# Optimization experiments

Hardware: AMD Instinct MI355X
Metric: run time of the kernel (lower is better)

Reference implementation:

```python
import jax, jax.numpy as jnp
import numpy as np


def setup_inputs() -> dict:
    key = jax.random.key(0)
    ks = jax.random.split(key, 5)
    B, C, D, H, W = 2, 256, 8, 28, 28
    mid = C // 2
    # Kaiming-normal-ish init (std = sqrt(2/fan_in)) for 1x1 conv weights
    def kaiming(k, shape, fan_in):
        return jax.random.normal(k, shape, dtype=jnp.float32) * np.sqrt(2.0 / fan_in)
    x = jax.random.normal(ks[0], (B, C, D, H, W), dtype=jnp.float32)
    w1 = kaiming(ks[1], (mid, C), C)
    w2 = kaiming(ks[2], (mid, C), C)
    w3 = kaiming(ks[3], (mid, C), C)
    w4 = kaiming(ks[4], (C, mid), mid)
    b1 = jnp.zeros((mid,), jnp.float32)
    b2 = jnp.zeros((mid,), jnp.float32)
    b3 = jnp.zeros((mid,), jnp.float32)
    b4 = jnp.zeros((C,), jnp.float32)
    return {"x": x, "w1": w1, "b1": b1, "w2": w2, "b2": b2,
            "w3": w3, "b3": b3, "w4": w4, "b4": b4}


def reference(x, w1, b1, w2, b2, w3, b3, w4, b4):
    # x: [B, C, D, H, W]; 1x1x1 Conv3d == channel matmul over flattened N = D*H*W
    B, C, D, H, W = x.shape
    N = D * H * W
    xf = x.reshape(B, C, N)                                   # [B, C, N]
    # theta: conv1 -> [B, N, mid]
    e1 = jnp.einsum('mc,bcn->bnm', w1, xf) + b1               # [B, N, mid]
    # phi: conv2 -> [B, mid, N]
    e2 = jnp.einsum('mc,bcn->bmn', w2, xf) + b2[:, None]      # [B, mid, N]
    # g: conv3 -> [B, N, mid]
    e3 = jnp.einsum('mc,bcn->bnm', w3, xf) + b3               # [B, N, mid]
    # unscaled attention: softmax over keys (last axis)
    kernel = jnp.einsum('bnm,bmk->bnk', e1, e2)               # [B, N, N]
    kernel = jax.nn.softmax(kernel, axis=2)
    attn = jnp.einsum('bnk,bkm->bnm', kernel, e3)             # [B, N, mid]
    # conv4 (1x1 Conv1d): mid -> C, applied on [B, mid, N]
    y = jnp.einsum('cm,bnm->bcn', w4, attn) + b4[:, None]     # [B, C, N]
    return x + y.reshape(B, C, D, H, W)
```

## Files before the change

### kernel.cpp

```cpp
#include <hip/hip_runtime.h>


#define BB  2
#define CC  256
#define NN  6272
#define MID 128

typedef _Float16 half4_t __attribute__((ext_vector_type(4)));
typedef _Float16 half8_t __attribute__((ext_vector_type(8)));
typedef float    floatx16 __attribute__((ext_vector_type(16)));

__device__ __forceinline__ void fma4(float4& a, const float4 v, const float s) {
    a.x += v.x * s; a.y += v.y * s; a.z += v.z * s; a.w += v.w * s;
}
__device__ __forceinline__ float dot4(const float4 a, const float4 b) {
    return a.x * b.x + a.y * b.y + a.z * b.z + a.w * b.w;
}

__global__ __launch_bounds__(256, 2) void proj_kernel(
    const float* __restrict__ x,
    const float* __restrict__ w1, const float* __restrict__ bi1,
    const float* __restrict__ w2, const float* __restrict__ bi2,
    const float* __restrict__ w3, const float* __restrict__ bi3,
    _Float16* __restrict__ Qg, _Float16* __restrict__ Kg, _Float16* __restrict__ VtG)
{
    const int t  = threadIdx.x;
    const int n0 = blockIdx.x * 64;
    const int pj = blockIdx.y;
    const int b  = blockIdx.z;
    const float* w  = (pj == 0) ? w1 : (pj == 1) ? w2 : w3;
    const float* bi = (pj == 0) ? bi1 : (pj == 1) ? bi2 : bi3;

    __shared__ float xs[CC * 68];
    {
        const float* xb = x + (size_t)b * CC * NN;
        for (int r = t; r < CC * 16; r += 256) {
            int c = r >> 4, j = (r & 15) << 2;
            float4 v = *(const float4*)(xb + (size_t)c * NN + n0 + j);
            *(float4*)&xs[c * 68 + j] = v;
        }
    }
    __syncthreads();

    const int n4 = (t & 15) << 2;
    const int m0 = (t >> 4) << 3;
    float4 acc4[8];
    #pragma unroll
    for (int k = 0; k < 8; ++k) acc4[k] = make_float4(0.f, 0.f, 0.f, 0.f);

    for (int cc = 0; cc < CC; cc += 4) {
        float4 xv[4];
        #pragma unroll
        for (int u = 0; u < 4; ++u)
            xv[u] = *(const float4*)&xs[(cc + u) * 68 + n4];
        #pragma unroll
        for (int k = 0; k < 8; ++k) {
            float4 wq = *(const float4*)(w + (size_t)(m0 + k) * CC + cc);
            fma4(acc4[k], xv[0], wq.x);
            fma4(acc4[k], xv[1], wq.y);
            fma4(acc4[k], xv[2], wq.z);
            fma4(acc4[k], xv[3], wq.w);
        }
    }

    const float* af = (const float*)acc4;
    float bb[8];
    #pragma unroll
    for (int k = 0; k < 8; ++k) bb[k] = bi[m0 + k];

    if (pj < 2) {
        _Float16* eo = ((pj == 0) ? Qg : Kg) + (size_t)b * NN * MID;
        #pragma unroll
        for (int i = 0; i < 4; ++i) {
            half8_t h;
            #pragma unroll
            for (int k = 0; k < 8; ++k) h[k] = (_Float16)(af[k * 4 + i] + bb[k]);
            *(half8_t*)(eo + (size_t)(n0 + n4 + i) * MID + m0) = h;
        }
    } else {
        _Float16* eo = VtG + (size_t)b * MID * NN;
        #pragma unroll
        for (int k = 0; k < 8; ++k) {
            half4_t h;
            #pragma unroll
            for (int i = 0; i < 4; ++i) h[i] = (_Float16)(af[k * 4 + i] + bb[k]);
            *(half4_t*)(eo + (size_t)(m0 + k) * NN + n0 + n4) = h;
        }
    }
}

__global__ __launch_bounds__(128, 2) void attn_kernel(
    const _Float16* __restrict__ Qg, const _Float16* __restrict__ Kg,
    const _Float16* __restrict__ VtG, float* __restrict__ attnW)
{
    const int t    = threadIdx.x;
    const int lane = t & 63;
    const int wave = t >> 6;
    const int l31  = lane & 31;
    const int l5   = lane >> 5;
    const int q0   = blockIdx.x * 32;
    const int b    = blockIdx.y;

    __shared__ __align__(16) char lds[40960];
    _Float16* Ks = (_Float16*)lds;
    _Float16* Vt = (_Float16*)(lds + 17408);
    _Float16* Pt = (_Float16*)(lds + 17408 + 18432);
    float* stats = (float*)(lds + 40448);
    float* Obuf  = (float*)lds;

    const _Float16* Qb = Qg + ((size_t)b * NN + q0) * MID;
    const _Float16* Kb = Kg + (size_t)b * NN * MID;
    const _Float16* Vb = VtG + (size_t)b * MID * NN;

    half8_t qf[8];
    #pragma unroll
    for (int ds = 0; ds < 8; ++ds)
        qf[ds] = *(const half8_t*)(Qb + (size_t)l31 * MID + ds * 16 + l5 * 8);

    floatx16 o[4];
    #pragma unroll
    for (int dt = 0; dt < 4; ++dt)
        #pragma unroll
        for (int j = 0; j < 16; ++j) o[dt][j] = 0.f;
    float m_run = -3.0e38f, l_run = 0.f;

    for (int kt = 0; kt < NN / 64; ++kt) {
        const int nk = kt * 64;
        #pragma unroll
        for (int it = 0; it < 8; ++it) {
            int c = it * 128 + t;
            int r = c >> 4, off = (c & 15) * 8;
            *(half8_t*)(Ks + r * 136 + off) =
                *(const half8_t*)(Kb + (size_t)(nk + r) * MID + off);
        }
        #pragma unroll
        for (int it = 0; it < 8; ++it) {
            int c = it * 128 + t;
            int d = c >> 3, off = (c & 7) * 8;
            *(half8_t*)(Vt + d * 72 + off) =
                *(const half8_t*)(Vb + (size_t)d * NN + nk + off);
        }
        __syncthreads();

        floatx16 s;
        #pragma unroll
        for (int j = 0; j < 16; ++j) s[j] = 0.f;
        const _Float16* krow = Ks + (wave * 32 + l31) * 136 + l5 * 8;
        #pragma unroll
        for (int ds = 0; ds < 8; ++ds)
            s = __builtin_amdgcn_mfma_f32_32x32x16_f16(
                    *(const half8_t*)(krow + ds * 16), qf[ds], s, 0, 0, 0);

        float tmax = s[0];
        #pragma unroll
        for (int j = 1; j < 16; ++j) tmax = fmaxf(tmax, s[j]);
        tmax = fmaxf(tmax, __shfl_xor(tmax, 32));
        const float m_new = fmaxf(m_run, tmax);
        const float alpha = __expf(m_run - m_new);
        m_run = m_new;

        float psum = 0.f;
        _Float16* prow = Pt + l31 * 72 + wave * 32 + 4 * l5;
        #pragma unroll
        for (int g = 0; g < 4; ++g) {
            float p0 = __expf(s[4 * g + 0] - m_new);
            float p1 = __expf(s[4 * g + 1] - m_new);
            float p2 = __expf(s[4 * g + 2] - m_new);
            float p3 = __expf(s[4 * g + 3] - m_new);
            psum += (p0 + p1) + (p2 + p3);
            half4_t h;
            h[0] = (_Float16)p0; h[1] = (_Float16)p1;
            h[2] = (_Float16)p2; h[3] = (_Float16)p3;
            *(half4_t*)(prow + 8 * g) = h;
        }
        psum += __shfl_xor(psum, 32);
        l_run = l_run * alpha + psum;

        #pragma unroll
        for (int dt = 0; dt < 4; ++dt)
            #pragma unroll
            for (int j = 0; j < 16; ++j) o[dt][j] *= alpha;

        __builtin_amdgcn_s_waitcnt(0xC07F);

        #pragma unroll
        for (int ks = 0; ks < 2; ++ks) {
            half8_t pf = *(const half8_t*)(Pt + l31 * 72 + wave * 32 + ks * 16 + l5 * 8);
            const _Float16* vcol = Vt + wave * 32 + ks * 16 + l5 * 8;
            #pragma unroll
            for (int dt = 0; dt < 4; ++dt)
                o[dt] = __builtin_amdgcn_mfma_f32_32x32x16_f16(
                            *(const half8_t*)(vcol + (dt * 32 + l31) * 72), pf,
                            o[dt], 0, 0, 0);
        }
        __syncthreads();
    }

    if (l5 == 0) {
        stats[wave * 64 + l31]      = m_run;
        stats[wave * 64 + 32 + l31] = l_run;
    }
    __syncthreads();
    const float m_o  = stats[(1 ^ wave) * 64 + l31];
    const float l_o  = stats[(1 ^ wave) * 64 + 32 + l31];
    const float m_st = fmaxf(m_run, m_o);
    const float sc   = __expf(m_run - m_st);
    const float l_st = l_run * sc + l_o * __expf(m_o - m_st);
    const float inv  = 1.0f / l_st;

    if (wave == 1) {
        #pragma unroll
        for (int dt = 0; dt < 4; ++dt)
            #pragma unroll
            for (int j = 0; j < 16; ++j) {
                int d = dt * 32 + (j & 3) + 8 * (j >> 2) + 4 * l5;
                Obuf[l31 * 132 + d] = o[dt][j] * sc;
            }
    }
    __syncthreads();
    if (wave == 0) {
        #pragma unroll
        for (int dt = 0; dt < 4; ++dt)
            #pragma unroll
            for (int j = 0; j < 16; ++j) {
                int d = dt * 32 + (j & 3) + 8 * (j >> 2) + 4 * l5;
                Obuf[l31 * 132 + d] = (Obuf[l31 * 132 + d] + o[dt][j] * sc) * inv;
            }
    }
    __syncthreads();
    #pragma unroll
    for (int it = 0; it < 8; ++it) {
        int c = it * 128 + t;
        int q = c >> 5, off = (c & 31) * 4;
        *(float4*)(attnW + ((size_t)b * NN + q0 + q) * MID + off) =
            *(const float4*)(Obuf + q * 132 + off);
    }
}

__global__ __launch_bounds__(256, 2) void epi_kernel(
    const float* __restrict__ attnW, const float* __restrict__ w4,
    const float* __restrict__ b4, const float* __restrict__ x,
    float* __restrict__ out)
{
    const int t  = threadIdx.x;
    const int n0 = blockIdx.x * 64;
    const int b  = blockIdx.y;

    __shared__ float as[64 * 132];
    for (int r = t; r < 64 * 32; r += 256) {
        int q = r >> 5, g = r & 31;
        float4 v = *(const float4*)(attnW + ((size_t)b * NN + (n0 + q)) * MID + (g << 2));
        *(float4*)&as[q * 132 + (g << 2)] = v;
    }
    __syncthreads();

    const int n4 = (t & 15) << 2;
    const int c0 = (t >> 4) << 4;
    float4 accE[16];
    #pragma unroll
    for (int k = 0; k < 16; ++k) accE[k] = make_float4(0.f, 0.f, 0.f, 0.f);

    for (int ms = 0; ms < 32; ++ms) {
        float4 av[4];
        #pragma unroll
        for (int i = 0; i < 4; ++i)
            av[i] = *(const float4*)&as[(n4 + i) * 132 + (ms << 2)];
        #pragma unroll
        for (int k = 0; k < 16; ++k) {
            float4 wq = *(const float4*)(w4 + (size_t)(c0 + k) * MID + (ms << 2));
            accE[k].x += dot4(av[0], wq);
            accE[k].y += dot4(av[1], wq);
            accE[k].z += dot4(av[2], wq);
            accE[k].w += dot4(av[3], wq);
        }
    }

    #pragma unroll
    for (int k = 0; k < 16; ++k) {
        const int c = c0 + k;
        const float bv = b4[c];
        const size_t off = ((size_t)b * CC + c) * NN + n0 + n4;
        float4 xr = *(const float4*)(x + off);
        float4 r;
        r.x = accE[k].x + bv + xr.x;
        r.y = accE[k].y + bv + xr.y;
        r.z = accE[k].z + bv + xr.z;
        r.w = accE[k].w + bv + xr.w;
        *(float4*)(out + off) = r;
    }
}

extern "C" void kernel_launch(void* const* d_in, const int* in_sizes, int n_in,
                              void* d_out, int out_size, void* d_ws, size_t ws_size,
                              hipStream_t stream)
{
    const float* x  = (const float*)d_in[0];
    const float* w1 = (const float*)d_in[1];
    const float* b1 = (const float*)d_in[2];
    const float* w2 = (const float*)d_in[3];
    const float* b2 = (const float*)d_in[4];
    const float* w3 = (const float*)d_in[5];
    const float* b3 = (const float*)d_in[6];
    const float* w4 = (const float*)d_in[7];
    const float* b4 = (const float*)d_in[8];
    float* out = (float*)d_out;

    _Float16* Qg  = (_Float16*)d_ws;
    _Float16* Kg  = Qg + (size_t)BB * NN * MID;
    _Float16* VtG = Kg + (size_t)BB * NN * MID;
    float* attnW  = (float*)(VtG + (size_t)BB * NN * MID);

    proj_kernel<<<dim3(NN / 64, 3, BB), 256, 0, stream>>>(x, w1, b1, w2, b2, w3, b3, Qg, Kg, VtG);
    attn_kernel<<<dim3(NN / 32, BB), 128, 0, stream>>>(Qg, Kg, VtG, attnW);
    epi_kernel<<<dim3(NN / 64, BB), 256, 0, stream>>>(attnW, w4, b4, x, out);
}
```

Baseline: 306.8 us.

## Split attention keys across blocks with a combine kernel and fp16 intermediates

Splits the key dimension of the attention kernel into four chunks, so the grid has four times as many blocks, and writes fp16 partial outputs plus per-row max and sum stats. A new combine kernel merges the partials. K is now read straight from global memory instead of through LDS, which shrinks LDS use so occupancy can rise, and the V/P LDS strides change. It also skips the rescale of the accumulator when the running max does not change, and stores the attention output in fp16 for the epilogue. This adds an extra kernel, the partial-output traffic (staged in the output buffer) and some fp16 rounding.

```diff
diff --git a/kernel.cpp b/kernel.cpp
--- a/kernel.cpp
+++ b/kernel.cpp
@@ -5,6 +5,8 @@
 #define CC  256
 #define NN  6272
 #define MID 128
+#define KS  4
+#define NT  (NN / 64)
 
 typedef _Float16 half4_t __attribute__((ext_vector_type(4)));
 typedef _Float16 half8_t __attribute__((ext_vector_type(8)));
@@ -89,9 +91,10 @@
     }
 }
 
-__global__ __launch_bounds__(128, 2) void attn_kernel(
+__global__ __launch_bounds__(128, 4) void attn_kernel(
     const _Float16* __restrict__ Qg, const _Float16* __restrict__ Kg,
-    const _Float16* __restrict__ VtG, float* __restrict__ attnW)
+    const _Float16* __restrict__ VtG, _Float16* __restrict__ Opart,
+    float* __restrict__ MLg)
 {
     const int t    = threadIdx.x;
     const int lane = t & 63;
@@ -99,13 +102,15 @@
     const int l31  = lane & 31;
     const int l5   = lane >> 5;
     const int q0   = blockIdx.x * 32;
-    const int b    = blockIdx.y;
-
-    __shared__ __align__(16) char lds[40960];
-    _Float16* Ks = (_Float16*)lds;
-    _Float16* Vt = (_Float16*)(lds + 17408);
-    _Float16* Pt = (_Float16*)(lds + 17408 + 18432);
-    float* stats = (float*)(lds + 40448);
+    const int sp   = blockIdx.y;
+    const int b    = blockIdx.z;
+    const int kt0  = (NT * sp) / KS;
+    const int kt1  = (NT * (sp + 1)) / KS;
+
+    __shared__ __align__(16) char lds[22272];
+    _Float16* Vt = (_Float16*)lds;
+    _Float16* Pt = (_Float16*)(lds + 17408);
+    float* stats = (float*)(lds + 21760);
     float* Obuf  = (float*)lds;
 
     const _Float16* Qb = Qg + ((size_t)b * NN + q0) * MID;
@@ -124,20 +129,13 @@
         for (int j = 0; j < 16; ++j) o[dt][j] = 0.f;
     float m_run = -3.0e38f, l_run = 0.f;
 
-    for (int kt = 0; kt < NN / 64; ++kt) {
+    for (int kt = kt0; kt < kt1; ++kt) {
         const int nk = kt * 64;
-        #pragma unroll
-        for (int it = 0; it < 8; ++it) {
-            int c = it * 128 + t;
-            int r = c >> 4, off = (c & 15) * 8;
-            *(half8_t*)(Ks + r * 136 + off) =
-                *(const half8_t*)(Kb + (size_t)(nk + r) * MID + off);
-        }
         #pragma unroll
         for (int it = 0; it < 8; ++it) {
             int c = it * 128 + t;
             int d = c >> 3, off = (c & 7) * 8;
-            *(half8_t*)(Vt + d * 72 + off) =
+            *(half8_t*)(Vt + d * 68 + off) =
                 *(const half8_t*)(Vb + (size_t)d * NN + nk + off);
         }
         __syncthreads();
@@ -145,7 +143,7 @@
         floatx16 s;
         #pragma unroll
         for (int j = 0; j < 16; ++j) s[j] = 0.f;
-        const _Float16* krow = Ks + (wave * 32 + l31) * 136 + l5 * 8;
+        const _Float16* krow = Kb + (size_t)(nk + wave * 32 + l31) * MID + l5 * 8;
         #pragma unroll
         for (int ds = 0; ds < 8; ++ds)
             s = __builtin_amdgcn_mfma_f32_32x32x16_f16(
@@ -155,18 +153,26 @@
         #pragma unroll
         for (int j = 1; j < 16; ++j) tmax = fmaxf(tmax, s[j]);
         tmax = fmaxf(tmax, __shfl_xor(tmax, 32));
-        const float m_new = fmaxf(m_run, tmax);
-        const float alpha = __expf(m_run - m_new);
-        m_run = m_new;
+
+        if (!__all(tmax <= m_run)) {
+            const float m_new = fmaxf(m_run, tmax);
+            const float alpha = __expf(m_run - m_new);
+            m_run = m_new;
+            l_run *= alpha;
+            #pragma unroll
+            for (int dt = 0; dt < 4; ++dt)
+                #pragma unroll
+                for (int j = 0; j < 16; ++j) o[dt][j] *= alpha;
+        }
 
         float psum = 0.f;
-        _Float16* prow = Pt + l31 * 72 + wave * 32 + 4 * l5;
+        _Float16* prow = Pt + l31 * 68 + wave * 32 + 4 * l5;
         #pragma unroll
         for (int g = 0; g < 4; ++g) {
-            float p0 = __expf(s[4 * g + 0] - m_new);
-            float p1 = __expf(s[4 * g + 1] - m_new);
-            float p2 = __expf(s[4 * g + 2] - m_new);
-            float p3 = __expf(s[4 * g + 3] - m_new);
+            float p0 = __expf(s[4 * g + 0] - m_run);
+            float p1 = __expf(s[4 * g + 1] - m_run);
+            float p2 = __expf(s[4 * g + 2] - m_run);
+            float p3 = __expf(s[4 * g + 3] - m_run);
             psum += (p0 + p1) + (p2 + p3);
             half4_t h;
             h[0] = (_Float16)p0; h[1] = (_Float16)p1;
@@ -174,23 +180,18 @@
             *(half4_t*)(prow + 8 * g) = h;
         }
         psum += __shfl_xor(psum, 32);
-        l_run = l_run * alpha + psum;
-
-        #pragma unroll
-        for (int dt = 0; dt < 4; ++dt)
-            #pragma unroll
-            for (int j = 0; j < 16; ++j) o[dt][j] *= alpha;
+        l_run += psum;
 
         __builtin_amdgcn_s_waitcnt(0xC07F);
 
         #pragma unroll
         for (int ks = 0; ks < 2; ++ks) {
-            half8_t pf = *(const half8_t*)(Pt + l31 * 72 + wave * 32 + ks * 16 + l5 * 8);
+            half8_t pf = *(const half8_t*)(Pt + l31 * 68 + wave * 32 + ks * 16 + l5 * 8);
             const _Float16* vcol = Vt + wave * 32 + ks * 16 + l5 * 8;
             #pragma unroll
             for (int dt = 0; dt < 4; ++dt)
                 o[dt] = __builtin_amdgcn_mfma_f32_32x32x16_f16(
-                            *(const half8_t*)(vcol + (dt * 32 + l31) * 72), pf,
+                            *(const half8_t*)(vcol + (dt * 32 + l31) * 68), pf,
                             o[dt], 0, 0, 0);
         }
         __syncthreads();
@@ -206,7 +207,12 @@
     const float m_st = fmaxf(m_run, m_o);
     const float sc   = __expf(m_run - m_st);
     const float l_st = l_run * sc + l_o * __expf(m_o - m_st);
-    const float inv  = 1.0f / l_st;
+
+    if (t < 32) {
+        float* mlb = MLg + ((size_t)(b * KS + sp) * 2) * NN + q0;
+        mlb[t]      = m_st;
+        mlb[NN + t] = l_st;
+    }
 
     if (wave == 1) {
         #pragma unroll
@@ -224,21 +230,71 @@
             #pragma unroll
             for (int j = 0; j < 16; ++j) {
                 int d = dt * 32 + (j & 3) + 8 * (j >> 2) + 4 * l5;
-                Obuf[l31 * 132 + d] = (Obuf[l31 * 132 + d] + o[dt][j] * sc) * inv;
+                Obuf[l31 * 132 + d] += o[dt][j] * sc;
             }
     }
     __syncthreads();
-    #pragma unroll
-    for (int it = 0; it < 8; ++it) {
+    _Float16* Ob = Opart + ((size_t)(b * KS + sp) * NN + q0) * MID;
+    #pragma unroll
+    for (int it = 0; it < 4; ++it) {
         int c = it * 128 + t;
-        int q = c >> 5, off = (c & 31) * 4;
-        *(float4*)(attnW + ((size_t)b * NN + q0 + q) * MID + off) =
-            *(const float4*)(Obuf + q * 132 + off);
-    }
+        int q = c >> 4, g = c & 15;
+        const float* src = &Obuf[q * 132 + g * 8];
+        half8_t h;
+        #pragma unroll
+        for (int j = 0; j < 8; ++j) h[j] = (_Float16)src[j];
+        *(half8_t*)(Ob + (size_t)q * MID + g * 8) = h;
+    }
+}
+
+__global__ __launch_bounds__(256, 4) void comb_kernel(
+    const _Float16* __restrict__ Opart, const float* __restrict__ MLg,
+    _Float16* __restrict__ attnW)
+{
+    const int t  = threadIdx.x;
+    const int b  = blockIdx.y;
+    const int q  = blockIdx.x * 32 + (t >> 3);
+    const int dg = (t & 7) * 16;
+
+    float mv[KS], lv[KS];
+    float m_g = -3.0e38f;
+    #pragma unroll
+    for (int s = 0; s < KS; ++s) {
+        const float* mlb = MLg + ((size_t)(b * KS + s) * 2) * NN;
+        mv[s] = mlb[q];
+        lv[s] = mlb[NN + q];
+        m_g = fmaxf(m_g, mv[s]);
+    }
+    float lg = 0.f, w[KS];
+    #pragma unroll
+    for (int s = 0; s < KS; ++s) { w[s] = __expf(mv[s] - m_g); lg += lv[s] * w[s]; }
+    const float inv = 1.0f / lg;
+
+    float acc[16];
+    #pragma unroll
+    for (int j = 0; j < 16; ++j) acc[j] = 0.f;
+    #pragma unroll
+    for (int s = 0; s < KS; ++s) {
+        const half8_t* Op = (const half8_t*)(Opart + ((size_t)(b * KS + s) * NN + q) * MID + dg);
+        half8_t v0 = Op[0], v1 = Op[1];
+        #pragma unroll
+        for (int j = 0; j < 8; ++j) {
+            acc[j]     += (float)v0[j] * w[s];
+            acc[8 + j] += (float)v1[j] * w[s];
+        }
+    }
+    half8_t h0, h1;
+    #pragma unroll
+    for (int j = 0; j < 8; ++j) {
+        h0[j] = (_Float16)(acc[j] * inv);
+        h1[j] = (_Float16)(acc[8 + j] * inv);
+    }
+    half8_t* Ow = (half8_t*)(attnW + ((size_t)b * NN + q) * MID + dg);
+    Ow[0] = h0; Ow[1] = h1;
 }
 
 __global__ __launch_bounds__(256, 2) void epi_kernel(
-    const float* __restrict__ attnW, const float* __restrict__ w4,
+    const _Float16* __restrict__ attnW, const float* __restrict__ w4,
     const float* __restrict__ b4, const float* __restrict__ x,
     float* __restrict__ out)
 {
@@ -247,10 +303,12 @@
     const int b  = blockIdx.y;
 
     __shared__ float as[64 * 132];
-    for (int r = t; r < 64 * 32; r += 256) {
-        int q = r >> 5, g = r & 31;
-        float4 v = *(const float4*)(attnW + ((size_t)b * NN + (n0 + q)) * MID + (g << 2));
-        *(float4*)&as[q * 132 + (g << 2)] = v;
+    for (int r = t; r < 64 * 16; r += 256) {
+        int q = r >> 4, g = r & 15;
+        half8_t v = *(const half8_t*)(attnW + ((size_t)b * NN + n0 + q) * MID + g * 8);
+        float* dst = &as[q * 132 + g * 8];
+        #pragma unroll
+        for (int j = 0; j < 8; ++j) dst[j] = (float)v[j];
     }
     __syncthreads();
 
@@ -305,12 +363,15 @@
     const float* b4 = (const float*)d_in[8];
     float* out = (float*)d_out;
 
-    _Float16* Qg  = (_Float16*)d_ws;
-    _Float16* Kg  = Qg + (size_t)BB * NN * MID;
-    _Float16* VtG = Kg + (size_t)BB * NN * MID;
-    float* attnW  = (float*)(VtG + (size_t)BB * NN * MID);
+    _Float16* Qg    = (_Float16*)d_ws;
+    _Float16* Kg    = Qg + (size_t)BB * NN * MID;
+    _Float16* VtG   = Kg + (size_t)BB * NN * MID;
+    _Float16* attnW = VtG + (size_t)BB * NN * MID;
+    float* MLg      = (float*)(attnW + (size_t)BB * NN * MID);
+    _Float16* Opart = (_Float16*)d_out;
 
     proj_kernel<<<dim3(NN / 64, 3, BB), 256, 0, stream>>>(x, w1, b1, w2, b2, w3, b3, Qg, Kg, VtG);
-    attn_kernel<<<dim3(NN / 32, BB), 128, 0, stream>>>(Qg, Kg, VtG, attnW);
+    attn_kernel<<<dim3(NN / 32, KS, BB), 128, 0, stream>>>(Qg, Kg, VtG, Opart, MLg);
+    comb_kernel<<<dim3(NN / 32, BB), 256, 0, stream>>>(Opart, MLg, attnW);
     epi_kernel<<<dim3(NN / 64, BB), 256, 0, stream>>>(attnW, w4, b4, x, out);
 }
```

Measured after the change: 385.1 us. +25.5%, slower.

## Prefetch next K/V tile into registers and pad LDS strides

Applied to the files above, without the earlier changes.

Global loads of the next K and V tiles are issued into registers before the current tile's MFMA work, then written to LDS at the start of the next iteration, so global latency overlaps compute. The V and P LDS row stride changes from 72 to 68 halves, shrinking LDS and altering the bank pattern. This costs extra VGPRs for the staging registers, and the 68-half stride leaves some 16-byte vector accesses only 8-byte aligned, which may split them. The final iteration reloads the last tile redundantly.

```diff
diff --git a/kernel.cpp b/kernel.cpp
--- a/kernel.cpp
+++ b/kernel.cpp
@@ -5,6 +5,7 @@
 #define CC  256
 #define NN  6272
 #define MID 128
+#define NT  (NN / 64)
 
 typedef _Float16 half4_t __attribute__((ext_vector_type(4)));
 typedef _Float16 half8_t __attribute__((ext_vector_type(8)));
@@ -101,11 +102,11 @@
     const int q0   = blockIdx.x * 32;
     const int b    = blockIdx.y;
 
-    __shared__ __align__(16) char lds[40960];
+    __shared__ __align__(16) char lds[39680];
     _Float16* Ks = (_Float16*)lds;
     _Float16* Vt = (_Float16*)(lds + 17408);
-    _Float16* Pt = (_Float16*)(lds + 17408 + 18432);
-    float* stats = (float*)(lds + 40448);
+    _Float16* Pt = (_Float16*)(lds + 34816);
+    float* stats = (float*)(lds + 39168);
     float* Obuf  = (float*)lds;
 
     const _Float16* Qb = Qg + ((size_t)b * NN + q0) * MID;
@@ -124,23 +125,32 @@
         for (int j = 0; j < 16; ++j) o[dt][j] = 0.f;
     float m_run = -3.0e38f, l_run = 0.f;
 
-    for (int kt = 0; kt < NN / 64; ++kt) {
+    const int kr   = t >> 4,  koff = (t & 15) * 8;
+    const int vd   = t >> 3,  voff = (t & 7) * 8;
+    half8_t kreg[8], vreg[8];
+
+    auto load_tile = [&](int nk) {
+        #pragma unroll
+        for (int it = 0; it < 8; ++it)
+            kreg[it] = *(const half8_t*)(Kb + (size_t)(nk + it * 8 + kr) * MID + koff);
+        #pragma unroll
+        for (int it = 0; it < 8; ++it)
+            vreg[it] = *(const half8_t*)(Vb + (size_t)(it * 16 + vd) * NN + nk + voff);
+    };
+    load_tile(0);
+
+    for (int kt = 0; kt < NT; ++kt) {
         const int nk = kt * 64;
-        #pragma unroll
-        for (int it = 0; it < 8; ++it) {
-            int c = it * 128 + t;
-            int r = c >> 4, off = (c & 15) * 8;
-            *(half8_t*)(Ks + r * 136 + off) =
-                *(const half8_t*)(Kb + (size_t)(nk + r) * MID + off);
-        }
-        #pragma unroll
-        for (int it = 0; it < 8; ++it) {
-            int c = it * 128 + t;
-            int d = c >> 3, off = (c & 7) * 8;
-            *(half8_t*)(Vt + d * 72 + off) =
-                *(const half8_t*)(Vb + (size_t)d * NN + nk + off);
-        }
         __syncthreads();
+        #pragma unroll
+        for (int it = 0; it < 8; ++it)
+            *(half8_t*)(Ks + (it * 8 + kr) * 136 + koff) = kreg[it];
+        #pragma unroll
+        for (int it = 0; it < 8; ++it)
+            *(half8_t*)(Vt + (it * 16 + vd) * 68 + voff) = vreg[it];
+        __syncthreads();
+
+        load_tile(kt + 1 < NT ? nk + 64 : nk);
 
         floatx16 s;
         #pragma unroll
@@ -160,7 +170,7 @@
         m_run = m_new;
 
         float psum = 0.f;
-        _Float16* prow = Pt + l31 * 72 + wave * 32 + 4 * l5;
+        _Float16* prow = Pt + l31 * 68 + wave * 32 + 4 * l5;
         #pragma unroll
         for (int g = 0; g < 4; ++g) {
             float p0 = __expf(s[4 * g + 0] - m_new);
@@ -185,17 +195,17 @@
 
         #pragma unroll
         for (int ks = 0; ks < 2; ++ks) {
-            half8_t pf = *(const half8_t*)(Pt + l31 * 72 + wave * 32 + ks * 16 + l5 * 8);
+            half8_t pf = *(const half8_t*)(Pt + l31 * 68 + wave * 32 + ks * 16 + l5 * 8);
             const _Float16* vcol = Vt + wave * 32 + ks * 16 + l5 * 8;
             #pragma unroll
             for (int dt = 0; dt < 4; ++dt)
                 o[dt] = __builtin_amdgcn_mfma_f32_32x32x16_f16(
-                            *(const half8_t*)(vcol + (dt * 32 + l31) * 72), pf,
+                            *(const half8_t*)(vcol + (dt * 32 + l31) * 68), pf,
                             o[dt], 0, 0, 0);
         }
-        __syncthreads();
-    }
-
+    }
+
+    __syncthreads();
     if (l5 == 0) {
         stats[wave * 64 + l31]      = m_run;
         stats[wave * 64 + 32 + l31] = l_run;
```

New measurement: 404.4 us. 1.32x slower.
